# Kernel tuning notes

Hardware: AMD Instinct MI355X
Metric: run time of the kernel (lower is better)

The kernel has to match this reference:

```python
import jax, jax.numpy as jnp
import numpy as np

EPS = 1e-07
NUM_ITERATIONS = 3

B, O, H, W, I, D = 8, 32, 14, 14, 32, 16


def squash(s, axis=-1):
    # squared norm over capsule dim
    sq = jnp.sum(s * s, axis=axis)                      # [..., ] norms
    safe = jnp.sqrt(sq + EPS)
    factor = sq / (1.0 + sq)
    return (factor / safe)[..., None] * s


def setup_inputs() -> dict:
    key = jax.random.key(0)
    k1, = jax.random.split(key, 1)
    preds = jax.random.normal(k1, (B, O, H, W, I, D), dtype=jnp.float32)
    b = jnp.zeros((1, O, H, W, I), dtype=jnp.float32)   # routing logits param
    return {"tensor_of_prediction_vector": preds, "b": b}


def reference(tensor_of_prediction_vector, b):
    preds = tensor_of_prediction_vector                 # [B,O,H,W,I,D]
    c = jax.nn.softmax(b, axis=-1)                      # [1,O,H,W,I]
    v = squash(jnp.sum(c[..., None] * preds, axis=-2))  # [B,O,H,W,D]
    b_batch = b
    for _ in range(NUM_ITERATIONS):
        # agreement: dot(pred, v) over capsule dim -> [B,O,H,W,I]
        b_batch = b_batch + jnp.sum(preds * v[..., None, :], axis=-1)
        c = jax.nn.softmax(b_batch, axis=-1)
        v = squash(jnp.sum(preds * c[..., None], axis=-2))
    return v
```

## Files before the change

### kernel.cpp

```cpp
#include <hip/hip_runtime.h>


#define EPSQ 1e-7f
#define LOG2E 1.442695041f

constexpr int NI = 32, ND = 16;
constexpr int SITES = 50176;
constexpr int OHW   = 6272;
constexpr int THREADS = 256;
constexpr int BLOCKS  = SITES / 32;

__device__ __forceinline__ float dpp1(float x) {
    return __int_as_float(__builtin_amdgcn_mov_dpp(__float_as_int(x), 0xB1, 0xF, 0xF, true));
}
__device__ __forceinline__ float dpp2(float x) {
    return __int_as_float(__builtin_amdgcn_mov_dpp(__float_as_int(x), 0x4E, 0xF, 0xF, true));
}
__device__ __forceinline__ float dpp4(float x) {
    return __int_as_float(__builtin_amdgcn_mov_dpp(__float_as_int(x), 0x141, 0xF, 0xF, true));
}
__device__ __forceinline__ float red8(float x) {
    x += dpp1(x); x += dpp2(x); x += dpp4(x); return x;
}
__device__ __forceinline__ void fma4(float4& a, float c, const float4& x) {
    a.x = fmaf(c, x.x, a.x); a.y = fmaf(c, x.y, a.y);
    a.z = fmaf(c, x.z, a.z); a.w = fmaf(c, x.w, a.w);
}
__device__ __forceinline__ float dot4(const float4& a, const float4& b) {
    return fmaf(a.x, b.x, fmaf(a.y, b.y, fmaf(a.z, b.z, a.w * b.w)));
}
__device__ __forceinline__ void red8_4(float4& a) {
    a.x += dpp1(a.x); a.y += dpp1(a.y); a.z += dpp1(a.z); a.w += dpp1(a.w);
    a.x += dpp2(a.x); a.y += dpp2(a.y); a.z += dpp2(a.z); a.w += dpp2(a.w);
    a.x += dpp4(a.x); a.y += dpp4(a.y); a.z += dpp4(a.z); a.w += dpp4(a.w);
}

__global__ __launch_bounds__(256, 4) void routing_kernel(
    const float* __restrict__ preds,
    const float* __restrict__ bparam,
    float* __restrict__ out)
{
    __shared__ float4 lds4[2048];
    const int tid  = threadIdx.x;
    const int lane = tid & 63;
    const int wib  = tid >> 6;
    const int wave = blockIdx.x * 4 + wib;
    const int g    = lane & 7;
    const int s_w  = lane >> 3;
    const int site = wave * 8 + s_w;

    float4* wlds = lds4 + wib * 512;
    const float4* pg = (const float4*)preds + (size_t)wave * 1024;

    const int sohw = site % OHW;
    const float4 bv = ((const float4*)bparam)[(size_t)sohw * 8 + g];

    float4 ta[8], tb[8];
    #pragma unroll
    for (int j = 0; j < 8; ++j) ta[j] = pg[j * 64 + lane];
    #pragma unroll
    for (int j = 0; j < 8; ++j) tb[j] = pg[512 + j * 64 + lane];

    auto write_phase = [&](int ph, const float4* t) {
        #pragma unroll
        for (int j = 0; j < 8; ++j) {
            const int x = j >> 1;
            const int k = ph * 4 + x;
            const int m = (j & 1) * 64 + lane;
            wlds[x * 128 + (m ^ k ^ (((j & 1) << 2)))] = t[j];
        }
    };

    float4 p[4][4];
    const int rkey = s_w ^ (g & 4);
    const int rbase = (s_w & 3) * 128 + 16 * g;

    write_phase(0, ta);
    asm volatile("s_waitcnt lgkmcnt(0)" ::: "memory");
    if (s_w < 4) {
        #pragma unroll
        for (int r = 0; r < 4; ++r)
            #pragma unroll
            for (int u = 0; u < 4; ++u)
                p[r][u] = wlds[(s_w & 3) * 128 + ((16 * g + 4 * r + u) ^ rkey)];
    }
    asm volatile("s_waitcnt lgkmcnt(0)" ::: "memory");
    write_phase(1, tb);
    asm volatile("s_waitcnt lgkmcnt(0)" ::: "memory");
    if (s_w >= 4) {
        #pragma unroll
        for (int r = 0; r < 4; ++r)
            #pragma unroll
            for (int u = 0; u < 4; ++u)
                p[r][u] = wlds[(s_w & 3) * 128 + ((16 * g + 4 * r + u) ^ rkey)];
    }

    float bl[4] = {bv.x * LOG2E, bv.y * LOG2E, bv.z * LOG2E, bv.w * LOG2E};

    float4 s0, s1, s2, s3;
    float  f;

    auto pass = [&]() {
        float e[4];
        float sm = 0.0f;
        #pragma unroll
        for (int k = 0; k < 4; ++k) { e[k] = __builtin_amdgcn_exp2f(bl[k]); sm += e[k]; }
        sm = red8(sm);
        const float r = __frcp_rn(sm);

        s0 = make_float4(0,0,0,0); s1 = make_float4(0,0,0,0);
        s2 = make_float4(0,0,0,0); s3 = make_float4(0,0,0,0);
        #pragma unroll
        for (int k = 0; k < 4; ++k) {
            fma4(s0, e[k], p[k][0]); fma4(s1, e[k], p[k][1]);
            fma4(s2, e[k], p[k][2]); fma4(s3, e[k], p[k][3]);
        }
        red8_4(s0); red8_4(s1); red8_4(s2); red8_4(s3);

        const float sqt = dot4(s0, s0) + dot4(s1, s1) + dot4(s2, s2) + dot4(s3, s3);
        const float sq  = r * r * sqt;
        f = sq * __frcp_rn(1.0f + sq) * __frsqrt_rn(sq + EPSQ) * r;
    };

    pass();

    #pragma unroll
    for (int it = 0; it < 3; ++it) {
        const float fl = f * LOG2E;
        #pragma unroll
        for (int k = 0; k < 4; ++k) {
            const float qk = dot4(p[k][0], s0) + dot4(p[k][1], s1)
                           + dot4(p[k][2], s2) + dot4(p[k][3], s3);
            bl[k] = fmaf(fl, qk, bl[k]);
        }
        pass();
    }

    if (g < 4) {
        float4 w = (g == 0) ? s0 : (g == 1) ? s1 : (g == 2) ? s2 : s3;
        w.x *= f; w.y *= f; w.z *= f; w.w *= f;
        ((float4*)out)[(size_t)site * 4 + g] = w;
    }
}

extern "C" void kernel_launch(void* const* d_in, const int* in_sizes, int n_in,
                              void* d_out, int out_size, void* d_ws, size_t ws_size,
                              hipStream_t stream) {
    const float* preds  = (const float*)d_in[0];
    const float* bparam = (const float*)d_in[1];
    float* out = (float*)d_out;
    routing_kernel<<<BLOCKS, THREADS, 0, stream>>>(preds, bparam, out);
}
```

Before: 32.50 us.

## Use direct global-to-LDS loads with 4 lanes per site and 8 capsules per lane

Each lane now holds 8 input capsules (4 lanes per site, 16 sites per wave) instead of 4 (8 lanes per site). The predictions are streamed through LDS in four phases using global_load_lds, which replaces the register-staged global loads and explicit LDS writes. Cross-lane reductions drop from three DPP steps to two, and every lane now takes part in the output store. In exchange, each thread holds more registers (p[8][4]), the occupancy hint drops from 4 to 3, and the phase barriers wait on vmcnt(0), which serializes the load and read phases.

Result: slower. 88.40 us (+172.0%).

```diff
diff --git a/kernel.cpp b/kernel.cpp
--- a/kernel.cpp
+++ b/kernel.cpp
@@ -4,23 +4,16 @@
 #define EPSQ 1e-7f
 #define LOG2E 1.442695041f
 
-constexpr int NI = 32, ND = 16;
+constexpr int OHW   = 6272;
 constexpr int SITES = 50176;
-constexpr int OHW   = 6272;
 constexpr int THREADS = 256;
-constexpr int BLOCKS  = SITES / 32;
+constexpr int BLOCKS  = SITES / 64;
 
 __device__ __forceinline__ float dpp1(float x) {
     return __int_as_float(__builtin_amdgcn_mov_dpp(__float_as_int(x), 0xB1, 0xF, 0xF, true));
 }
 __device__ __forceinline__ float dpp2(float x) {
     return __int_as_float(__builtin_amdgcn_mov_dpp(__float_as_int(x), 0x4E, 0xF, 0xF, true));
-}
-__device__ __forceinline__ float dpp4(float x) {
-    return __int_as_float(__builtin_amdgcn_mov_dpp(__float_as_int(x), 0x141, 0xF, 0xF, true));
-}
-__device__ __forceinline__ float red8(float x) {
-    x += dpp1(x); x += dpp2(x); x += dpp4(x); return x;
 }
 __device__ __forceinline__ void fma4(float4& a, float c, const float4& x) {
     a.x = fmaf(c, x.x, a.x); a.y = fmaf(c, x.y, a.y);
@@ -29,13 +22,18 @@
 __device__ __forceinline__ float dot4(const float4& a, const float4& b) {
     return fmaf(a.x, b.x, fmaf(a.y, b.y, fmaf(a.z, b.z, a.w * b.w)));
 }
-__device__ __forceinline__ void red8_4(float4& a) {
+__device__ __forceinline__ void qred4(float4& a) {
     a.x += dpp1(a.x); a.y += dpp1(a.y); a.z += dpp1(a.z); a.w += dpp1(a.w);
     a.x += dpp2(a.x); a.y += dpp2(a.y); a.z += dpp2(a.z); a.w += dpp2(a.w);
-    a.x += dpp4(a.x); a.y += dpp4(a.y); a.z += dpp4(a.z); a.w += dpp4(a.w);
 }
 
-__global__ __launch_bounds__(256, 4) void routing_kernel(
+__device__ __forceinline__ void gload16(const float4* g, float4* l) {
+    __builtin_amdgcn_global_load_lds(
+        (const __attribute__((address_space(1))) void*)g,
+        (__attribute__((address_space(3))) void*)l, 16, 0, 0);
+}
+
+__global__ __launch_bounds__(256, 3) void routing_kernel(
     const float* __restrict__ preds,
     const float* __restrict__ bparam,
     float* __restrict__ out)
@@ -45,77 +43,70 @@
     const int lane = tid & 63;
     const int wib  = tid >> 6;
     const int wave = blockIdx.x * 4 + wib;
-    const int g    = lane & 7;
-    const int s_w  = lane >> 3;
-    const int site = wave * 8 + s_w;
+    const int q    = lane & 3;
+    const int s_w  = lane >> 2;
+    const int site = wave * 16 + s_w;
 
     float4* wlds = lds4 + wib * 512;
-    const float4* pg = (const float4*)preds + (size_t)wave * 1024;
+    const float4* pg = (const float4*)preds + (size_t)wave * 2048;
+
+    const int hi  = lane >> 5;
+    const int w32 = lane & 31;
+    int soff[8];
+    #pragma unroll
+    for (int t = 0; t < 8; ++t) {
+        const int x = 2 * t + hi;
+        soff[t] = x * 128 + (w32 ^ (x & 7));
+    }
+
+    #pragma unroll
+    for (int t = 0; t < 8; ++t) gload16(pg + soff[t], wlds + t * 64);
 
     const int sohw = site % OHW;
-    const float4 bv = ((const float4*)bparam)[(size_t)sohw * 8 + g];
+    const float* bs = bparam + (size_t)sohw * 32 + q;
+    float bl[8];
+    #pragma unroll
+    for (int k = 0; k < 8; ++k) bl[k] = bs[4 * k] * LOG2E;
 
-    float4 ta[8], tb[8];
+    float4 p[8][4];
+    const int rbase = s_w * 32;
+    const int rkey  = s_w & 7;
     #pragma unroll
-    for (int j = 0; j < 8; ++j) ta[j] = pg[j * 64 + lane];
-    #pragma unroll
-    for (int j = 0; j < 8; ++j) tb[j] = pg[512 + j * 64 + lane];
-
-    auto write_phase = [&](int ph, const float4* t) {
+    for (int ph = 0; ph < 4; ++ph) {
+        asm volatile("s_waitcnt vmcnt(0)" ::: "memory");
         #pragma unroll
-        for (int j = 0; j < 8; ++j) {
-            const int x = j >> 1;
-            const int k = ph * 4 + x;
-            const int m = (j & 1) * 64 + lane;
-            wlds[x * 128 + (m ^ k ^ (((j & 1) << 2)))] = t[j];
-        }
-    };
-
-    float4 p[4][4];
-    const int rkey = s_w ^ (g & 4);
-    const int rbase = (s_w & 3) * 128 + 16 * g;
-
-    write_phase(0, ta);
-    asm volatile("s_waitcnt lgkmcnt(0)" ::: "memory");
-    if (s_w < 4) {
-        #pragma unroll
-        for (int r = 0; r < 4; ++r)
+        for (int m = 0; m < 2; ++m) {
+            const int j = q + 4 * m;
             #pragma unroll
             for (int u = 0; u < 4; ++u)
-                p[r][u] = wlds[(s_w & 3) * 128 + ((16 * g + 4 * r + u) ^ rkey)];
+                p[2 * ph + m][u] = wlds[rbase + ((j * 4 + u) ^ rkey)];
+        }
+        if (ph < 3) {
+            asm volatile("s_waitcnt lgkmcnt(0)" ::: "memory");
+            #pragma unroll
+            for (int t = 0; t < 8; ++t)
+                gload16(pg + (soff[t] + 32 * (ph + 1)), wlds + t * 64);
+        }
     }
-    asm volatile("s_waitcnt lgkmcnt(0)" ::: "memory");
-    write_phase(1, tb);
-    asm volatile("s_waitcnt lgkmcnt(0)" ::: "memory");
-    if (s_w >= 4) {
-        #pragma unroll
-        for (int r = 0; r < 4; ++r)
-            #pragma unroll
-            for (int u = 0; u < 4; ++u)
-                p[r][u] = wlds[(s_w & 3) * 128 + ((16 * g + 4 * r + u) ^ rkey)];
-    }
-
-    float bl[4] = {bv.x * LOG2E, bv.y * LOG2E, bv.z * LOG2E, bv.w * LOG2E};
 
     float4 s0, s1, s2, s3;
     float  f;
 
     auto pass = [&]() {
-        float e[4];
         float sm = 0.0f;
-        #pragma unroll
-        for (int k = 0; k < 4; ++k) { e[k] = __builtin_amdgcn_exp2f(bl[k]); sm += e[k]; }
-        sm = red8(sm);
-        const float r = __frcp_rn(sm);
-
         s0 = make_float4(0,0,0,0); s1 = make_float4(0,0,0,0);
         s2 = make_float4(0,0,0,0); s3 = make_float4(0,0,0,0);
         #pragma unroll
-        for (int k = 0; k < 4; ++k) {
-            fma4(s0, e[k], p[k][0]); fma4(s1, e[k], p[k][1]);
-            fma4(s2, e[k], p[k][2]); fma4(s3, e[k], p[k][3]);
+        for (int k = 0; k < 8; ++k) {
+            const float e = __builtin_amdgcn_exp2f(bl[k]);
+            sm += e;
+            fma4(s0, e, p[k][0]); fma4(s1, e, p[k][1]);
+            fma4(s2, e, p[k][2]); fma4(s3, e, p[k][3]);
         }
-        red8_4(s0); red8_4(s1); red8_4(s2); red8_4(s3);
+        sm += dpp1(sm);
+        sm += dpp2(sm);
+        const float r = __frcp_rn(sm);
+        qred4(s0); qred4(s1); qred4(s2); qred4(s3);
 
         const float sqt = dot4(s0, s0) + dot4(s1, s1) + dot4(s2, s2) + dot4(s3, s3);
         const float sq  = r * r * sqt;
@@ -128,7 +119,7 @@
     for (int it = 0; it < 3; ++it) {
         const float fl = f * LOG2E;
         #pragma unroll
-        for (int k = 0; k < 4; ++k) {
+        for (int k = 0; k < 8; ++k) {
             const float qk = dot4(p[k][0], s0) + dot4(p[k][1], s1)
                            + dot4(p[k][2], s2) + dot4(p[k][3], s3);
             bl[k] = fmaf(fl, qk, bl[k]);
@@ -136,11 +127,9 @@
         pass();
     }
 
-    if (g < 4) {
-        float4 w = (g == 0) ? s0 : (g == 1) ? s1 : (g == 2) ? s2 : s3;
-        w.x *= f; w.y *= f; w.z *= f; w.w *= f;
-        ((float4*)out)[(size_t)site * 4 + g] = w;
-    }
+    float4 w = (q == 0) ? s0 : (q == 1) ? s1 : (q == 2) ? s2 : s3;
+    w.x *= f; w.y *= f; w.z *= f; w.w *= f;
+    ((float4*)out)[(size_t)wave * 64 + lane] = w;
 }
 
 extern "C" void kernel_launch(void* const* d_in, const int* in_sizes, int n_in,
```
